# Performance work log

Hardware: AMD Instinct MI355X
Metric: run time of the kernel (lower is better)

Reference implementation:

```python
import jax, jax.numpy as jnp
import numpy as np

def binarize(t):
    # deterministic sign binarization to {-1, +1}
    return jnp.where(t >= 0, 1.0, -1.0).astype(t.dtype)

def setup_inputs() -> dict:
    key = jax.random.key(0)
    k1, k2 = jax.random.split(key)
    x = jax.random.normal(k1, (8192, 4096), dtype=jnp.float32)
    kernel = jax.random.normal(k2, (4096, 4096), dtype=jnp.float32)
    return {"x": x, "kernel": kernel}

def reference(x, kernel):
    # BinaryLayer.call with binary=True: matmul(binarize(x), binarize(W))
    return jnp.matmul(binarize(x), binarize(kernel))
```

## Files before the change

kernel.cpp:

```cpp
#include <hip/hip_runtime.h>
#include <stdint.h>

#define MDIM 8192
#define NDIM 4096
#define KDIM 4096
#define KB2  (KDIM / 2)
#define BKB  64
#define NT   (KDIM / 128)

#define BM 256
#define BN 256
#define BUFSZ 32768

typedef __attribute__((ext_vector_type(4))) int   i32x4;
typedef __attribute__((ext_vector_type(8))) int   i32x8;
typedef __attribute__((ext_vector_type(4))) float f32x4;

__device__ __forceinline__ void gload16(const void* g, void* l) {
    __builtin_amdgcn_global_load_lds(
        (const __attribute__((address_space(1))) void*)g,
        (__attribute__((address_space(3))) void*)l, 16, 0, 0);
}

__device__ __forceinline__ i32x8 pad8(i32x4 v) {
    i32x8 r;
    r[0] = v[0]; r[1] = v[1]; r[2] = v[2]; r[3] = v[3];
    r[4] = 0;    r[5] = 0;    r[6] = 0;    r[7] = 0;
    return r;
}

#define MFMA_FP4(a, b, c)                                                   \
    __builtin_amdgcn_mfma_scale_f32_16x16x128_f8f6f4(                        \
        (a), (b), (c), 4, 4, 0, 0x7F7F7F7F, 0, 0x7F7F7F7F)

__global__ __launch_bounds__(256) void pack_a4_kernel(const float* __restrict__ X,
                                                      uint8_t* __restrict__ A4) {
    size_t gt = (size_t)blockIdx.x * 256 + threadIdx.x;
    const float4* x4 = (const float4*)X + gt * 4;
    uint32_t out[2] = {0, 0};
#pragma unroll
    for (int q = 0; q < 4; ++q) {
        float4 v = x4[q];
        uint32_t b0 = (v.x >= 0.f ? 0x2u : 0xAu) | ((v.y >= 0.f ? 0x2u : 0xAu) << 4);
        uint32_t b1 = (v.z >= 0.f ? 0x2u : 0xAu) | ((v.w >= 0.f ? 0x2u : 0xAu) << 4);
        out[q >> 1] |= (b0 | (b1 << 8)) << ((q & 1) * 16);
    }
    ((uint2*)A4)[gt] = make_uint2(out[0], out[1]);
}

__global__ __launch_bounds__(256) void pack_b4t_kernel(const float* __restrict__ W,
                                                       uint8_t* __restrict__ B4) {
    __shared__ uint8_t t[64][72];
    const int tid = threadIdx.x;
    const int k0 = blockIdx.y * 64, n0 = blockIdx.x * 64;
#pragma unroll
    for (int r = 0; r < 4; ++r) {
        int e  = r * 1024 + tid * 4;
        int k  = e >> 6;
        int nn = e & 63;
        float4 v = *(const float4*)&W[(size_t)(k0 + k) * NDIM + n0 + nn];
        uint32_t b0 = (v.x >= 0.f) ? 0x2u : 0xAu;
        uint32_t b1 = (v.y >= 0.f) ? 0x2u : 0xAu;
        uint32_t b2 = (v.z >= 0.f) ? 0x2u : 0xAu;
        uint32_t b3 = (v.w >= 0.f) ? 0x2u : 0xAu;
        *(uint32_t*)&t[k][nn] = b0 | (b1 << 8) | (b2 << 16) | (b3 << 24);
    }
    __syncthreads();
    const int n = tid >> 2, kc = tid & 3;
    uint32_t w[2] = {0, 0};
#pragma unroll
    for (int b = 0; b < 8; ++b) {
        int k = kc * 16 + b * 2;
        uint32_t byte = (uint32_t)t[k][n] | ((uint32_t)t[k + 1][n] << 4);
        w[b >> 2] |= byte << ((b & 3) * 8);
    }
    *(uint2*)&B4[(size_t)(n0 + n) * KB2 + k0 / 2 + kc * 8] = make_uint2(w[0], w[1]);
}

__global__ __launch_bounds__(512, 2) void binmm_fp4_kernel(const uint8_t* __restrict__ A4,
                                                           const uint8_t* __restrict__ B4,
                                                           float* __restrict__ C) {
    __shared__ uint8_t lds[4 * BUFSZ];

    const int tid = threadIdx.x, lane = tid & 63, wid = tid >> 6;
    const int wr = wid >> 2, wc = wid & 3;
    const int l15 = lane & 15, g = (lane >> 4) & 3;
    const int m0 = blockIdx.y * BM, n0 = blockIdx.x * BN;

    const int srowp = tid >> 2;
    const int fS    = (tid >> 3) & 3;
    const int csrc  = ((tid & 3) ^ fS) * 16;
    const uint8_t* pA0 = A4 + (size_t)(m0 + srowp)       * KB2 + csrc;
    const uint8_t* pA1 = A4 + (size_t)(m0 + 128 + srowp) * KB2 + csrc;
    const uint8_t* pB0 = B4 + (size_t)(n0 + srowp)       * KB2 + csrc;
    const uint8_t* pB1 = B4 + (size_t)(n0 + 128 + srowp) * KB2 + csrc;

#define STAGE(bufOff) do {                                                     \
        gload16(pA0, lds + (bufOff) + tid * 16);                               \
        gload16(pA1, lds + (bufOff) + 8192  + tid * 16);                       \
        gload16(pB0, lds + (bufOff) + 16384 + tid * 16);                       \
        gload16(pB1, lds + (bufOff) + 24576 + tid * 16);                       \
        pA0 += BKB; pA1 += BKB; pB0 += BKB; pB1 += BKB;                        \
    } while (0)

    const int fR = (l15 >> 1) & 3;
    const int aBase = (wr * 128 + l15) * 64 + ((g ^ fR) * 16);
    const int bBase = 16384 + (wc * 64 + l15) * 64 + ((g ^ fR) * 16);

    f32x4 acc[8][4];
#pragma unroll
    for (int m = 0; m < 8; ++m)
#pragma unroll
        for (int n = 0; n < 4; ++n) acc[m][n] = (f32x4){0.f, 0.f, 0.f, 0.f};

#define COMPUTE(bufOff) do {                                                   \
        const uint8_t* bp_ = lds + (bufOff);                                   \
        i32x8 b8_0 = pad8(*(const i32x4*)(bp_ + bBase));                       \
        i32x8 b8_1 = pad8(*(const i32x4*)(bp_ + bBase + 1024));                \
        i32x8 b8_2 = pad8(*(const i32x4*)(bp_ + bBase + 2048));                \
        i32x8 b8_3 = pad8(*(const i32x4*)(bp_ + bBase + 3072));                \
        i32x4 aN = *(const i32x4*)(bp_ + aBase);                               \
        __builtin_amdgcn_s_setprio(1);                                         \
        _Pragma("unroll")                                                      \
        for (int mf = 0; mf < 8; ++mf) {                                       \
            i32x8 a8 = pad8(aN);                                               \
            if (mf < 7) aN = *(const i32x4*)(bp_ + aBase + (mf + 1) * 1024);   \
            acc[mf][0] = MFMA_FP4(a8, b8_0, acc[mf][0]);                       \
            acc[mf][1] = MFMA_FP4(a8, b8_1, acc[mf][1]);                       \
            acc[mf][2] = MFMA_FP4(a8, b8_2, acc[mf][2]);                       \
            acc[mf][3] = MFMA_FP4(a8, b8_3, acc[mf][3]);                       \
        }                                                                      \
        __builtin_amdgcn_s_setprio(0);                                         \
    } while (0)

#define SYNC(n) do {                                                           \
        __builtin_amdgcn_sched_barrier(0);                                     \
        asm volatile("s_waitcnt vmcnt(" #n ")" ::: "memory");                  \
        __builtin_amdgcn_s_barrier();                                          \
        __builtin_amdgcn_sched_barrier(0);                                     \
    } while (0)

    STAGE(0);
    STAGE(BUFSZ);
    STAGE(2 * BUFSZ);
    SYNC(8);

#pragma unroll 1
    for (int t = 0; t < NT - 3; ++t) {
        STAGE(((t + 3) & 3) * BUFSZ);
        COMPUTE((t & 3) * BUFSZ);
        SYNC(8);
    }
    COMPUTE(1 * BUFSZ);
    SYNC(4);
    COMPUTE(2 * BUFSZ);
    SYNC(0);
    COMPUTE(3 * BUFSZ);

#pragma unroll
    for (int mf = 0; mf < 8; ++mf) {
#pragma unroll
        for (int nf = 0; nf < 4; ++nf) {
            size_t cc = (size_t)(n0 + wc * 64 + nf * 16 + l15);
            int rbase = m0 + wr * 128 + mf * 16 + g * 4;
#pragma unroll
            for (int reg = 0; reg < 4; ++reg)
                C[(size_t)(rbase + reg) * NDIM + cc] = acc[mf][nf][reg];
        }
    }
#undef STAGE
#undef COMPUTE
#undef SYNC
}

extern "C" void kernel_launch(void* const* d_in, const int* in_sizes, int n_in,
                              void* d_out, int out_size, void* d_ws, size_t ws_size,
                              hipStream_t stream) {
    const float* x = (const float*)d_in[0];
    const float* w = (const float*)d_in[1];
    float* out = (float*)d_out;

    uint8_t* A4 = (uint8_t*)d_ws;
    uint8_t* B4 = (uint8_t*)d_ws + (size_t)MDIM * KB2;

    pack_a4_kernel<<<(int)((size_t)MDIM * KDIM / 16 / 256), 256, 0, stream>>>(x, A4);
    pack_b4t_kernel<<<dim3(NDIM / 64, KDIM / 64), 256, 0, stream>>>(w, B4);
    binmm_fp4_kernel<<<dim3(NDIM / BN, MDIM / BM), 512, 0, stream>>>(A4, B4, out);
}
```

Measured before the change: 126.0 us.

## Split each K-tile into two phases interleaving LDS reads, global staging and MFMAs

Each K-tile is now processed in two halves of four M-fragments. Before each half, all of that half's LDS fragment reads are issued, followed by half of the next tile's global-to-LDS loads. Workgroup barriers and an lgkmcnt(0) wait separate these from a dense block of MFMAs run at raised priority. The aim is a ping-pong schedule where waves alternate between memory and matrix work, so loads overlap better with compute. The cost is extra barriers per tile, and the full LDS-read wait before the MFMAs removes the earlier fine-grained interleaving of A loads with MFMAs.

```diff
diff --git a/kernel.cpp b/kernel.cpp
--- a/kernel.cpp
+++ b/kernel.cpp
@@ -95,12 +95,15 @@
     const uint8_t* pB0 = B4 + (size_t)(n0 + srowp)       * KB2 + csrc;
     const uint8_t* pB1 = B4 + (size_t)(n0 + 128 + srowp) * KB2 + csrc;
 
-#define STAGE(bufOff) do {                                                     \
+#define STAGE_A(bufOff) do {                                                   \
         gload16(pA0, lds + (bufOff) + tid * 16);                               \
         gload16(pA1, lds + (bufOff) + 8192  + tid * 16);                       \
+        pA0 += BKB; pA1 += BKB;                                                \
+    } while (0)
+#define STAGE_B(bufOff) do {                                                   \
         gload16(pB0, lds + (bufOff) + 16384 + tid * 16);                       \
         gload16(pB1, lds + (bufOff) + 24576 + tid * 16);                       \
-        pA0 += BKB; pA1 += BKB; pB0 += BKB; pB1 += BKB;                        \
+        pB0 += BKB; pB1 += BKB;                                                \
     } while (0)
 
     const int fR = (l15 >> 1) & 3;
@@ -113,49 +116,76 @@
 #pragma unroll
         for (int n = 0; n < 4; ++n) acc[m][n] = (f32x4){0.f, 0.f, 0.f, 0.f};
 
-#define COMPUTE(bufOff) do {                                                   \
-        const uint8_t* bp_ = lds + (bufOff);                                   \
-        i32x8 b8_0 = pad8(*(const i32x4*)(bp_ + bBase));                       \
-        i32x8 b8_1 = pad8(*(const i32x4*)(bp_ + bBase + 1024));                \
-        i32x8 b8_2 = pad8(*(const i32x4*)(bp_ + bBase + 2048));                \
-        i32x8 b8_3 = pad8(*(const i32x4*)(bp_ + bBase + 3072));                \
-        i32x4 aN = *(const i32x4*)(bp_ + aBase);                               \
+#define TILE(cur, nxt, DO_STAGE) do {                                          \
+        const uint8_t* bp_ = lds + (cur);                                      \
+        i32x4 bF[4], aF[4];                                                    \
+             \
+        _Pragma("unroll")                                                      \
+        for (int nf = 0; nf < 4; ++nf)                                         \
+            bF[nf] = *(const i32x4*)(bp_ + bBase + nf * 1024);                 \
+        _Pragma("unroll")                                                      \
+        for (int mf = 0; mf < 4; ++mf)                                         \
+            aF[mf] = *(const i32x4*)(bp_ + aBase + mf * 1024);                 \
+        if (DO_STAGE) STAGE_A(nxt);                                            \
+        __builtin_amdgcn_sched_barrier(0);                                     \
+        __builtin_amdgcn_s_barrier();                                          \
+        asm volatile("s_waitcnt lgkmcnt(0)" ::: "memory");                     \
+        __builtin_amdgcn_sched_barrier(0);                                     \
         __builtin_amdgcn_s_setprio(1);                                         \
         _Pragma("unroll")                                                      \
-        for (int mf = 0; mf < 8; ++mf) {                                       \
-            i32x8 a8 = pad8(aN);                                               \
-            if (mf < 7) aN = *(const i32x4*)(bp_ + aBase + (mf + 1) * 1024);   \
-            acc[mf][0] = MFMA_FP4(a8, b8_0, acc[mf][0]);                       \
-            acc[mf][1] = MFMA_FP4(a8, b8_1, acc[mf][1]);                       \
-            acc[mf][2] = MFMA_FP4(a8, b8_2, acc[mf][2]);                       \
-            acc[mf][3] = MFMA_FP4(a8, b8_3, acc[mf][3]);                       \
+        for (int mf = 0; mf < 4; ++mf) {                                       \
+            i32x8 a8 = pad8(aF[mf]);                                           \
+            acc[mf][0] = MFMA_FP4(a8, pad8(bF[0]), acc[mf][0]);                \
+            acc[mf][1] = MFMA_FP4(a8, pad8(bF[1]), acc[mf][1]);                \
+            acc[mf][2] = MFMA_FP4(a8, pad8(bF[2]), acc[mf][2]);                \
+            acc[mf][3] = MFMA_FP4(a8, pad8(bF[3]), acc[mf][3]);                \
         }                                                                      \
         __builtin_amdgcn_s_setprio(0);                                         \
+        __builtin_amdgcn_sched_barrier(0);                                     \
+        __builtin_amdgcn_s_barrier();                                          \
+                 \
+        _Pragma("unroll")                                                      \
+        for (int mf = 0; mf < 4; ++mf)                                         \
+            aF[mf] = *(const i32x4*)(bp_ + aBase + (4 + mf) * 1024);           \
+        if (DO_STAGE) STAGE_B(nxt);                                            \
+        __builtin_amdgcn_sched_barrier(0);                                     \
+        __builtin_amdgcn_s_barrier();                                          \
+        asm volatile("s_waitcnt lgkmcnt(0)" ::: "memory");                     \
+        __builtin_amdgcn_sched_barrier(0);                                     \
+        __builtin_amdgcn_s_setprio(1);                                         \
+        _Pragma("unroll")                                                      \
+        for (int mf = 0; mf < 4; ++mf) {                                       \
+            i32x8 a8 = pad8(aF[mf]);                                           \
+            acc[4 + mf][0] = MFMA_FP4(a8, pad8(bF[0]), acc[4 + mf][0]);        \
+            acc[4 + mf][1] = MFMA_FP4(a8, pad8(bF[1]), acc[4 + mf][1]);        \
+            acc[4 + mf][2] = MFMA_FP4(a8, pad8(bF[2]), acc[4 + mf][2]);        \
+            acc[4 + mf][3] = MFMA_FP4(a8, pad8(bF[3]), acc[4 + mf][3]);        \
+        }                                                                      \
+        __builtin_amdgcn_s_setprio(0);                                         \
+        __builtin_amdgcn_sched_barrier(0);                                     \
     } while (0)
 
 #define SYNC(n) do {                                                           \
-        __builtin_amdgcn_sched_barrier(0);                                     \
         asm volatile("s_waitcnt vmcnt(" #n ")" ::: "memory");                  \
         __builtin_amdgcn_s_barrier();                                          \
         __builtin_amdgcn_sched_barrier(0);                                     \
     } while (0)
 
-    STAGE(0);
-    STAGE(BUFSZ);
-    STAGE(2 * BUFSZ);
+    STAGE_A(0);          STAGE_B(0);
+    STAGE_A(BUFSZ);      STAGE_B(BUFSZ);
+    STAGE_A(2 * BUFSZ);  STAGE_B(2 * BUFSZ);
     SYNC(8);
 
 #pragma unroll 1
     for (int t = 0; t < NT - 3; ++t) {
-        STAGE(((t + 3) & 3) * BUFSZ);
-        COMPUTE((t & 3) * BUFSZ);
+        TILE((t & 3) * BUFSZ, ((t + 3) & 3) * BUFSZ, true);
         SYNC(8);
     }
-    COMPUTE(1 * BUFSZ);
+    TILE(1 * BUFSZ, 0, false);
     SYNC(4);
-    COMPUTE(2 * BUFSZ);
+    TILE(2 * BUFSZ, 0, false);
     SYNC(0);
-    COMPUTE(3 * BUFSZ);
+    TILE(3 * BUFSZ, 0, false);
 
 #pragma unroll
     for (int mf = 0; mf < 8; ++mf) {
@@ -168,8 +198,9 @@
                 C[(size_t)(rbase + reg) * NDIM + cc] = acc[mf][nf][reg];
         }
     }
-#undef STAGE
-#undef COMPUTE
+#undef STAGE_A
+#undef STAGE_B
+#undef TILE
 #undef SYNC
 }
 
```

New measurement: 127.2 us. About the same (+0.9%).

## Pre-tile packed FP4 operands and switch to 32x32x64 scaled MFMA

Applied to the files above, without the earlier changes.

The packing kernels now write A and B in a tile-contiguous layout (panel, k-tile, slot, row), so each GEMM stage copies one contiguous 16 KB block per operand instead of strided rows with an XOR swizzle. The GEMM moves from 16x16x128 to 32x32x64 FP4 MFMAs with 16-wide accumulators, which cuts LDS fragment reads per FLOP. The pack kernels also process more elements per thread. The new LDS read pattern (consecutive 16-byte rows) may cause bank conflicts without the swizzle, and the fragment and output mapping for the 32x32 instruction must match the hardware layout for results to be correct.

```diff
diff --git a/kernel.cpp b/kernel.cpp
--- a/kernel.cpp
+++ b/kernel.cpp
@@ -4,17 +4,16 @@
 #define MDIM 8192
 #define NDIM 4096
 #define KDIM 4096
-#define KB2  (KDIM / 2)
-#define BKB  64
 #define NT   (KDIM / 128)
+#define TILEB 16384
 
 #define BM 256
 #define BN 256
 #define BUFSZ 32768
 
-typedef __attribute__((ext_vector_type(4))) int   i32x4;
-typedef __attribute__((ext_vector_type(8))) int   i32x8;
-typedef __attribute__((ext_vector_type(4))) float f32x4;
+typedef __attribute__((ext_vector_type(4)))  int   i32x4;
+typedef __attribute__((ext_vector_type(8)))  int   i32x8;
+typedef __attribute__((ext_vector_type(16))) float f32x16;
 
 __device__ __forceinline__ void gload16(const void* g, void* l) {
     __builtin_amdgcn_global_load_lds(
@@ -29,107 +28,108 @@
     return r;
 }
 
-#define MFMA_FP4(a, b, c)                                                   \
-    __builtin_amdgcn_mfma_scale_f32_16x16x128_f8f6f4(                        \
+#define MFMA_FP4_32(a, b, c)                                                 \
+    __builtin_amdgcn_mfma_scale_f32_32x32x64_f8f6f4(                          \
         (a), (b), (c), 4, 4, 0, 0x7F7F7F7F, 0, 0x7F7F7F7F)
 
 __global__ __launch_bounds__(256) void pack_a4_kernel(const float* __restrict__ X,
-                                                      uint8_t* __restrict__ A4) {
-    size_t gt = (size_t)blockIdx.x * 256 + threadIdx.x;
-    const float4* x4 = (const float4*)X + gt * 4;
-    uint32_t out[2] = {0, 0};
+                                                      uint8_t* __restrict__ A4p) {
+    int tg    = blockIdx.x * 256 + threadIdx.x;
+    int row   = tg & 255;
+    int slot  = (tg >> 8) & 3;
+    int kt    = (tg >> 10) & 31;
+    int panel = tg >> 15;
+    const float4* src = (const float4*)(X + (size_t)(panel * 256 + row) * KDIM
+                                          + kt * 128 + slot * 32);
+    uint32_t w[4];
 #pragma unroll
     for (int q = 0; q < 4; ++q) {
-        float4 v = x4[q];
-        uint32_t b0 = (v.x >= 0.f ? 0x2u : 0xAu) | ((v.y >= 0.f ? 0x2u : 0xAu) << 4);
-        uint32_t b1 = (v.z >= 0.f ? 0x2u : 0xAu) | ((v.w >= 0.f ? 0x2u : 0xAu) << 4);
-        out[q >> 1] |= (b0 | (b1 << 8)) << ((q & 1) * 16);
+        float4 a = src[q * 2], b = src[q * 2 + 1];
+        w[q] = (a.x >= 0.f ? 0x2u : 0xAu)        | ((a.y >= 0.f ? 0x2u : 0xAu) << 4)
+             | ((a.z >= 0.f ? 0x2u : 0xAu) << 8) | ((a.w >= 0.f ? 0x2u : 0xAu) << 12)
+             | ((b.x >= 0.f ? 0x2u : 0xAu) << 16)| ((b.y >= 0.f ? 0x2u : 0xAu) << 20)
+             | ((b.z >= 0.f ? 0x2u : 0xAu) << 24)| ((b.w >= 0.f ? 0x2u : 0xAu) << 28);
     }
-    ((uint2*)A4)[gt] = make_uint2(out[0], out[1]);
+    ((uint4*)A4p)[tg] = make_uint4(w[0], w[1], w[2], w[3]);
 }
 
 __global__ __launch_bounds__(256) void pack_b4t_kernel(const float* __restrict__ W,
-                                                       uint8_t* __restrict__ B4) {
-    __shared__ uint8_t t[64][72];
-    const int tid = threadIdx.x;
-    const int k0 = blockIdx.y * 64, n0 = blockIdx.x * 64;
+                                                       uint8_t* __restrict__ B4p) {
+    __shared__ uint8_t P[64 * 80];
+    const int t  = threadIdx.x;
+    const int n0 = blockIdx.x * 64;
+    const int k0 = blockIdx.y * 128;
+    const int nt = t & 15, ks = t >> 4;
+    uint32_t a0 = 0, a1 = 0, a2 = 0, a3 = 0;
 #pragma unroll
-    for (int r = 0; r < 4; ++r) {
-        int e  = r * 1024 + tid * 4;
-        int k  = e >> 6;
-        int nn = e & 63;
-        float4 v = *(const float4*)&W[(size_t)(k0 + k) * NDIM + n0 + nn];
-        uint32_t b0 = (v.x >= 0.f) ? 0x2u : 0xAu;
-        uint32_t b1 = (v.y >= 0.f) ? 0x2u : 0xAu;
-        uint32_t b2 = (v.z >= 0.f) ? 0x2u : 0xAu;
-        uint32_t b3 = (v.w >= 0.f) ? 0x2u : 0xAu;
-        *(uint32_t*)&t[k][nn] = b0 | (b1 << 8) | (b2 << 16) | (b3 << 24);
+    for (int j = 0; j < 8; ++j) {
+        float4 v = *(const float4*)&W[(size_t)(k0 + ks * 8 + j) * NDIM + n0 + nt * 4];
+        int sh = (j >> 1) * 8 + (j & 1) * 4;
+        a0 |= (v.x >= 0.f ? 0x2u : 0xAu) << sh;
+        a1 |= (v.y >= 0.f ? 0x2u : 0xAu) << sh;
+        a2 |= (v.z >= 0.f ? 0x2u : 0xAu) << sh;
+        a3 |= (v.w >= 0.f ? 0x2u : 0xAu) << sh;
     }
+    *(uint32_t*)&P[(nt * 4 + 0) * 80 + ks * 4] = a0;
+    *(uint32_t*)&P[(nt * 4 + 1) * 80 + ks * 4] = a1;
+    *(uint32_t*)&P[(nt * 4 + 2) * 80 + ks * 4] = a2;
+    *(uint32_t*)&P[(nt * 4 + 3) * 80 + ks * 4] = a3;
     __syncthreads();
-    const int n = tid >> 2, kc = tid & 3;
-    uint32_t w[2] = {0, 0};
-#pragma unroll
-    for (int b = 0; b < 8; ++b) {
-        int k = kc * 16 + b * 2;
-        uint32_t byte = (uint32_t)t[k][n] | ((uint32_t)t[k + 1][n] << 4);
-        w[b >> 2] |= byte << ((b & 3) * 8);
-    }
-    *(uint2*)&B4[(size_t)(n0 + n) * KB2 + k0 / 2 + kc * 8] = make_uint2(w[0], w[1]);
+    const int n = t >> 2, slot = t & 3;
+    uint4 val = *(const uint4*)&P[n * 80 + slot * 16];
+    const int pn = (n0 + n) >> 8, rn = (n0 + n) & 255;
+    size_t addr = ((((size_t)pn * 32 + blockIdx.y) * 4 + slot) * 256 + rn) * 16;
+    *(uint4*)&B4p[addr] = val;
 }
 
-__global__ __launch_bounds__(512, 2) void binmm_fp4_kernel(const uint8_t* __restrict__ A4,
-                                                           const uint8_t* __restrict__ B4,
+__global__ __launch_bounds__(512, 2) void binmm_fp4_kernel(const uint8_t* __restrict__ A4p,
+                                                           const uint8_t* __restrict__ B4p,
                                                            float* __restrict__ C) {
     __shared__ uint8_t lds[4 * BUFSZ];
 
     const int tid = threadIdx.x, lane = tid & 63, wid = tid >> 6;
     const int wr = wid >> 2, wc = wid & 3;
-    const int l15 = lane & 15, g = (lane >> 4) & 3;
+    const int l31 = lane & 31, kh = lane >> 5;
     const int m0 = blockIdx.y * BM, n0 = blockIdx.x * BN;
 
-    const int srowp = tid >> 2;
-    const int fS    = (tid >> 3) & 3;
-    const int csrc  = ((tid & 3) ^ fS) * 16;
-    const uint8_t* pA0 = A4 + (size_t)(m0 + srowp)       * KB2 + csrc;
-    const uint8_t* pA1 = A4 + (size_t)(m0 + 128 + srowp) * KB2 + csrc;
-    const uint8_t* pB0 = B4 + (size_t)(n0 + srowp)       * KB2 + csrc;
-    const uint8_t* pB1 = B4 + (size_t)(n0 + 128 + srowp) * KB2 + csrc;
+    const uint8_t* pA = A4p + (size_t)blockIdx.y * 32 * TILEB + tid * 16;
+    const uint8_t* pB = B4p + (size_t)blockIdx.x * 32 * TILEB + tid * 16;
 
-#define STAGE(bufOff) do {                                                     \
-        gload16(pA0, lds + (bufOff) + tid * 16);                               \
-        gload16(pA1, lds + (bufOff) + 8192  + tid * 16);                       \
-        gload16(pB0, lds + (bufOff) + 16384 + tid * 16);                       \
-        gload16(pB1, lds + (bufOff) + 24576 + tid * 16);                       \
-        pA0 += BKB; pA1 += BKB; pB0 += BKB; pB1 += BKB;                        \
+#define STAGE(bufOff, t) do {                                                  \
+        gload16(pA + (t) * TILEB,        lds + (bufOff) + tid * 16);           \
+        gload16(pA + (t) * TILEB + 8192, lds + (bufOff) + 8192  + tid * 16);   \
+        gload16(pB + (t) * TILEB,        lds + (bufOff) + 16384 + tid * 16);   \
+        gload16(pB + (t) * TILEB + 8192, lds + (bufOff) + 24576 + tid * 16);   \
     } while (0)
 
-    const int fR = (l15 >> 1) & 3;
-    const int aBase = (wr * 128 + l15) * 64 + ((g ^ fR) * 16);
-    const int bBase = 16384 + (wc * 64 + l15) * 64 + ((g ^ fR) * 16);
+    const int aBase = kh * 4096 + (wr * 128 + l31) * 16;
+    const int bBase = 16384 + kh * 4096 + (wc * 64 + l31) * 16;
 
-    f32x4 acc[8][4];
+    f32x16 acc[4][2];
 #pragma unroll
-    for (int m = 0; m < 8; ++m)
+    for (int m = 0; m < 4; ++m)
 #pragma unroll
-        for (int n = 0; n < 4; ++n) acc[m][n] = (f32x4){0.f, 0.f, 0.f, 0.f};
+        for (int n = 0; n < 2; ++n)
+#pragma unroll
+            for (int e = 0; e < 16; ++e) acc[m][n][e] = 0.f;
 
 #define COMPUTE(bufOff) do {                                                   \
         const uint8_t* bp_ = lds + (bufOff);                                   \
-        i32x8 b8_0 = pad8(*(const i32x4*)(bp_ + bBase));                       \
-        i32x8 b8_1 = pad8(*(const i32x4*)(bp_ + bBase + 1024));                \
-        i32x8 b8_2 = pad8(*(const i32x4*)(bp_ + bBase + 2048));                \
-        i32x8 b8_3 = pad8(*(const i32x4*)(bp_ + bBase + 3072));                \
-        i32x4 aN = *(const i32x4*)(bp_ + aBase);                               \
+        i32x8 bF[2][2];                                                        \
+        _Pragma("unroll")                                                      \
+        for (int nf = 0; nf < 2; ++nf)                                         \
+            _Pragma("unroll")                                                  \
+            for (int s = 0; s < 2; ++s)                                        \
+                bF[nf][s] = pad8(*(const i32x4*)(bp_ + bBase + nf * 512 + s * 8192)); \
         __builtin_amdgcn_s_setprio(1);                                         \
         _Pragma("unroll")                                                      \
-        for (int mf = 0; mf < 8; ++mf) {                                       \
-            i32x8 a8 = pad8(aN);                                               \
-            if (mf < 7) aN = *(const i32x4*)(bp_ + aBase + (mf + 1) * 1024);   \
-            acc[mf][0] = MFMA_FP4(a8, b8_0, acc[mf][0]);                       \
-            acc[mf][1] = MFMA_FP4(a8, b8_1, acc[mf][1]);                       \
-            acc[mf][2] = MFMA_FP4(a8, b8_2, acc[mf][2]);                       \
-            acc[mf][3] = MFMA_FP4(a8, b8_3, acc[mf][3]);                       \
-        }                                                                      \
+        for (int s = 0; s < 2; ++s)                                            \
+            _Pragma("unroll")                                                  \
+            for (int mf = 0; mf < 4; ++mf) {                                   \
+                i32x8 a8 = pad8(*(const i32x4*)(bp_ + aBase + mf * 512 + s * 8192)); \
+                acc[mf][0] = MFMA_FP4_32(a8, bF[0][s], acc[mf][0]);            \
+                acc[mf][1] = MFMA_FP4_32(a8, bF[1][s], acc[mf][1]);            \
+            }                                                                  \
         __builtin_amdgcn_s_setprio(0);                                         \
     } while (0)
 
@@ -140,14 +140,14 @@
         __builtin_amdgcn_sched_barrier(0);                                     \
     } while (0)
 
-    STAGE(0);
-    STAGE(BUFSZ);
-    STAGE(2 * BUFSZ);
+    STAGE(0, 0);
+    STAGE(BUFSZ, 1);
+    STAGE(2 * BUFSZ, 2);
     SYNC(8);
 
 #pragma unroll 1
     for (int t = 0; t < NT - 3; ++t) {
-        STAGE(((t + 3) & 3) * BUFSZ);
+        STAGE(((t + 3) & 3) * BUFSZ, t + 3);
         COMPUTE((t & 3) * BUFSZ);
         SYNC(8);
     }
@@ -158,14 +158,16 @@
     COMPUTE(3 * BUFSZ);
 
 #pragma unroll
-    for (int mf = 0; mf < 8; ++mf) {
+    for (int mf = 0; mf < 4; ++mf) {
 #pragma unroll
-        for (int nf = 0; nf < 4; ++nf) {
-            size_t cc = (size_t)(n0 + wc * 64 + nf * 16 + l15);
-            int rbase = m0 + wr * 128 + mf * 16 + g * 4;
+        for (int nf = 0; nf < 2; ++nf) {
+            size_t cc = (size_t)(n0 + wc * 64 + nf * 32 + l31);
+            int rbase = m0 + wr * 128 + mf * 32 + 4 * kh;
 #pragma unroll
-            for (int reg = 0; reg < 4; ++reg)
-                C[(size_t)(rbase + reg) * NDIM + cc] = acc[mf][nf][reg];
+            for (int reg = 0; reg < 16; ++reg) {
+                int rr = (reg & 3) + 8 * (reg >> 2);
+                C[(size_t)(rbase + rr) * NDIM + cc] = acc[mf][nf][reg];
+            }
         }
     }
 #undef STAGE
@@ -180,10 +182,10 @@
     const float* w = (const float*)d_in[1];
     float* out = (float*)d_out;
 
-    uint8_t* A4 = (uint8_t*)d_ws;
-    uint8_t* B4 = (uint8_t*)d_ws + (size_t)MDIM * KB2;
+    uint8_t* A4p = (uint8_t*)d_ws;
+    uint8_t* B4p = (uint8_t*)d_ws + (size_t)MDIM * (KDIM / 2);
 
-    pack_a4_kernel<<<(int)((size_t)MDIM * KDIM / 16 / 256), 256, 0, stream>>>(x, A4);
-    pack_b4t_kernel<<<dim3(NDIM / 64, KDIM / 64), 256, 0, stream>>>(w, B4);
-    binmm_fp4_kernel<<<dim3(NDIM / BN, MDIM / BM), 512, 0, stream>>>(A4, B4, out);
+    pack_a4_kernel<<<(int)((size_t)MDIM * KDIM / 32 / 256), 256, 0, stream>>>(x, A4p);
+    pack_b4t_kernel<<<dim3(NDIM / 64, KDIM / 128), 256, 0, stream>>>(w, B4p);
+    binmm_fp4_kernel<<<dim3(NDIM / BN, MDIM / BM), 512, 0, stream>>>(A4p, B4p, out);
 }
```

New measurement: 135.5 us. +7.5%, slower.
